# Kernel optimization log

Hardware: AMD Instinct MI355X
Metric: run time of the kernel (lower is better)

Reference implementation:

```python
import jax, jax.numpy as jnp
import numpy as np

B, L, A, K = 2, 1024, 14, 30
NUM_RBF = 16
NPE = 16  # num_positional_embeddings
EF = 128  # edge_features
EDGE_IN = NPE + NUM_RBF * A * A  # 3152


def setup_inputs() -> dict:
    key = jax.random.key(0)
    ks = jax.random.split(key, 4)
    # coords scaled so pairwise distances span the RBF range [0, 20]
    X = jax.random.normal(ks[0], (B, L, A, 3), dtype=jnp.float32) * 3.0
    mask = jnp.ones((B, L), dtype=jnp.float32)
    residue_idx = jnp.tile(jnp.arange(L, dtype=jnp.int32)[None, :], (B, 1))
    chain_labels = jnp.zeros((B, L), dtype=jnp.int32)
    atom_mask = jax.random.randint(ks[1], (B, L, A), 0, 2).astype(jnp.float32)
    W_edge = jax.random.normal(ks[2], (EF, EDGE_IN), dtype=jnp.float32) * 0.02
    ln_gamma = jnp.ones((EF,), dtype=jnp.float32)
    ln_beta = jnp.zeros((EF,), dtype=jnp.float32)
    return {"X": X, "mask": mask, "residue_idx": residue_idx,
            "chain_labels": chain_labels, "atom_mask": atom_mask,
            "W_edge": W_edge, "ln_gamma": ln_gamma, "ln_beta": ln_beta}


def reference(X, mask, residue_idx, chain_labels, atom_mask, W_edge, ln_gamma, ln_beta):
    Bq, Lq = X.shape[0], X.shape[1]
    # ---- CA pairwise distances + masked top-k (smallest) ----
    X_ca = X[:, :, 1, :]
    m2 = mask[:, :, None] * mask[:, None, :]                    # [B,L,L]
    dX = X_ca[:, :, None, :] - X_ca[:, None, :, :]
    D = m2 * jnp.sqrt(jnp.sum(dX ** 2, -1) + 1e-6)
    D_max = jnp.max(D, -1, keepdims=True)
    D_adjust = D + 2.0 * (1.0 - m2) * D_max
    _, E_idx = jax.lax.top_k(-D_adjust, K)                      # smallest K -> [B,L,K]
    # ---- transformer positional encoding of relative index ----
    ii = jnp.arange(Lq, dtype=jnp.float32)[None, :, None]
    d = (E_idx.astype(jnp.float32) - ii)[..., None]             # [B,L,K,1]
    freq = jnp.exp(jnp.arange(0, NPE, 2, dtype=jnp.float32) * (-(np.log(10000.0) / NPE)))
    angles = d * freq                                           # [B,L,K,NPE/2]
    E_pos = jnp.concatenate([jnp.cos(angles), jnp.sin(angles)], -1)  # [B,L,K,NPE]
    # ---- impute CB, build 14-atom set ----
    N_, Ca, C_, O_ = X[:, :, 0, :], X[:, :, 1, :], X[:, :, 2, :], X[:, :, 3, :]
    b = Ca - N_
    c = C_ - Ca
    a = jnp.cross(b, c)
    Cb = -0.58273431 * a + 0.56802827 * b - 0.54067466 * c + Ca
    X2 = jnp.concatenate([jnp.stack([N_, Ca, C_, O_, Cb], -2), X[:, :, 5:, :]], -2)  # [B,L,14,3]
    am = 1.0 - atom_mask                                        # module passes 1 - atom_mask
    # ---- gather neighbor atoms, fused 14x14 atom-pair RBFs ----
    bidx = jnp.arange(Bq)[:, None, None]
    X2n = X2[bidx, E_idx]                                       # [B,L,K,14,3]
    amn = am[bidx, E_idx]                                       # [B,L,K,14]
    diff = X2[:, :, None, :, None, :] - X2n[:, :, :, None, :, :]
    Dab = jnp.sqrt(jnp.sum(diff ** 2, -1) + 1e-6)               # [B,L,K,14,14] (a of i, b of nbr)
    combo = am[:, :, None, :, None] * amn[:, :, :, None, :]     # [B,L,K,14,14]
    mu = jnp.linspace(0.0, 20.0, NUM_RBF)
    sigma = 20.0 / NUM_RBF
    rbf = jnp.exp(-(((Dab[..., None] - mu) / sigma) ** 2)) * combo[..., None]
    RBF_all = rbf.reshape(Bq, Lq, K, A * A * NUM_RBF)           # matches torch cat order (i,j,rbf)
    # ---- edge embedding + layernorm ----
    E = jnp.concatenate([E_pos, RBF_all], -1)                   # [B,L,K,EDGE_IN]
    E = E @ W_edge.T                                            # [B,L,K,EF]
    mean = jnp.mean(E, -1, keepdims=True)
    var = jnp.var(E, -1, keepdims=True)
    E = (E - mean) / jnp.sqrt(var + 1e-5) * ln_gamma + ln_beta
    return (E, E_idx)
```

## Files before the change

kernel.cpp:

```cpp
#include <hip/hip_runtime.h>
#include <hip/hip_bf16.h>
#include <stdint.h>

#define LQ 1024
#define BQ 2
#define AQ 14
#define KQ 30
#define EFQ 128
#define EDGE_IN 3152
#define KPAD 3200
#define NCHUNK 50
#define MTILE 128
#define ROWS (BQ*LQ*KQ)
#define EIDX_OFF (ROWS*EFQ)

typedef __attribute__((ext_vector_type(8))) _Float16 half8;
typedef __attribute__((ext_vector_type(2))) _Float16 half2t;
typedef __attribute__((ext_vector_type(4))) float floatx4;
typedef unsigned long long ull;

static __device__ __forceinline__ uint32_t pkh(float a, float b) {
    auto h = __builtin_amdgcn_cvt_pkrtz(a, b);
    return __builtin_bit_cast(uint32_t, h);
}
static __device__ __forceinline__ ull umin64(ull a, ull b) { return a < b ? a : b; }

__global__ __launch_bounds__(512) void topk_kernel(
    const float* __restrict__ X, const float* __restrict__ mask,
    const float* __restrict__ W, float* __restrict__ out,
    int* __restrict__ idx_ws, _Float16* __restrict__ wpad)
{
    __shared__ float xs[LQ], ys[LQ], zs[LQ], ms[LQ];
    const int t = threadIdx.x;

    if (blockIdx.x >= 256) {
        int base = (blockIdx.x - 256)*8192 + t;
        #pragma unroll
        for (int r = 0; r < 16; ++r) {
            int idx = base + r*512;
            int n = idx / KPAD, f = idx - n*KPAD;
            float v = (f < EDGE_IN) ? W[(size_t)n*EDGE_IN + f] : 0.0f;
            wpad[idx] = (_Float16)v;
        }
        return;
    }

    const int w = t >> 6, lane = t & 63;
    const int row = blockIdx.x*8 + w;
    const int b = row >> 10, i = row & (LQ - 1);

    for (int j = t; j < LQ; j += 512) {
        size_t base = ((size_t)(b*LQ + j))*42 + 3;
        xs[j] = X[base+0]; ys[j] = X[base+1]; zs[j] = X[base+2];
        ms[j] = mask[b*LQ + j];
    }
    __syncthreads();

    const float mif = ms[i];
    const double cx = (double)xs[i], cy = (double)ys[i], cz = (double)zs[i];

    double Dk[16]; float mf[16];
    bool allone = (mif == 1.0f);
    #pragma unroll
    for (int s = 0; s < 16; ++s) {
        int j = s*64 + lane;
        double dx = __dsub_rn(cx, (double)xs[j]);
        double dy = __dsub_rn(cy, (double)ys[j]);
        double dz = __dsub_rn(cz, (double)zs[j]);
        mf[s] = ms[j];
        Dk[s] = __dadd_rn(__dadd_rn(__dmul_rn(dx,dx), __dmul_rn(dy,dy)),
                          __dmul_rn(dz,dz));
        allone = allone && (mf[s] == 1.0f);
    }

    if (!__all(allone ? 1 : 0)) {
        const double mi_d = (double)mif;
        double lm = 0.0;
        #pragma unroll
        for (int s = 0; s < 16; ++s) {
            double m2 = __dmul_rn(mi_d, (double)mf[s]);
            Dk[s] = __dmul_rn(m2, sqrt(__dadd_rn(Dk[s], 1e-6)));
            lm = fmax(lm, Dk[s]);
        }
        #pragma unroll
        for (int off = 32; off; off >>= 1) lm = fmax(lm, __shfl_xor(lm, off));
        #pragma unroll
        for (int s = 0; s < 16; ++s) {
            double m2 = __dmul_rn(mi_d, (double)mf[s]);
            Dk[s] = __dadd_rn(Dk[s],
                    __dmul_rn(__dmul_rn(2.0, __dsub_rn(1.0, m2)), lm));
        }
    }

    ull key[16];
    #pragma unroll
    for (int s = 0; s < 16; ++s)
        key[s] = (((ull)__double_as_longlong(Dk[s])) & ~1023ull)
               | (unsigned)(s*64 + lane);

    for (int k = 0; k < KQ; ++k) {
        ull a0 = umin64(key[0],  key[1]),  a1 = umin64(key[2],  key[3]);
        ull a2 = umin64(key[4],  key[5]),  a3 = umin64(key[6],  key[7]);
        ull a4 = umin64(key[8],  key[9]),  a5 = umin64(key[10], key[11]);
        ull a6 = umin64(key[12], key[13]), a7 = umin64(key[14], key[15]);
        ull b0 = umin64(a0, a1), b1 = umin64(a2, a3);
        ull b2 = umin64(a4, a5), b3 = umin64(a6, a7);
        ull bk = umin64(umin64(b0, b1), umin64(b2, b3));
        #pragma unroll
        for (int off = 32; off; off >>= 1)
            bk = umin64(bk, (ull)__shfl_xor(bk, off));
        int j = (int)(bk & 1023ull);
        if (lane == 0) {
            int rg = row*KQ + k;
            idx_ws[rg] = j;
            out[EIDX_OFF + rg] = (float)j;
        }
        bool mine = ((j & 63) == lane);
        int s_win = j >> 6;
        #pragma unroll
        for (int s = 0; s < 16; ++s)
            key[s] = (mine && s == s_win) ? ~0ull : key[s];
    }
}

struct FusedSmem {
    alignas(16) unsigned short atoms[256*56];
    alignas(16) unsigned short Bl[128*64];
    alignas(16) float drow[MTILE];
    int residg[256];
    unsigned int maskb[256];
    float gsh[EFQ], bsh[EFQ];
};

static __device__ __forceinline__ void gen8(
    const unsigned short* __restrict__ atomsA,
    const unsigned short* __restrict__ atomsB,
    unsigned maskA, unsigned maskB, float drowv,
    int f0, uint32_t* __restrict__ v)
{
    if (f0 >= 16) {
        int p = (f0 - 16) >> 4;
        int rbase = (f0 - 16) & 15;
        int pc = p > 195 ? 195 : p;
        int a  = (pc * 74899) >> 20;
        int bp = pc - a*14;
        bool dead = (p > 195) |
                    ((((maskA >> a) | (maskB >> bp)) & 1u) != 0u);
        half2t c0 = *reinterpret_cast<const half2t*>(atomsA + a*4);
        half2t c1 = *reinterpret_cast<const half2t*>(atomsA + a*4 + 2);
        half2t n0 = *reinterpret_cast<const half2t*>(atomsB + bp*4);
        half2t n1 = *reinterpret_cast<const half2t*>(atomsB + bp*4 + 2);
        half2t dxy = c0 - n0;
        half2t dzw = c1 - n1;
        float dx = (float)dxy[0], dy = (float)dxy[1], dz = (float)dzw[0];
        float u = __builtin_amdgcn_sqrtf(dx*dx + dy*dy + dz*dz + 1e-6f) * 0.96089846f;
        u = dead ? 1.0e4f : u;
        #pragma unroll
        for (int k = 0; k < 4; ++k) {
            float t0 = __fmaf_rn(-(float)(rbase + 2*k),     1.28119795f, u);
            float t1 = __fmaf_rn(-(float)(rbase + 2*k + 1), 1.28119795f, u);
            v[k] = pkh(__builtin_amdgcn_exp2f(-(t0*t0)),
                       __builtin_amdgcn_exp2f(-(t1*t1)));
        }
    } else {
        const float fr[8] = {1.0f, 0.31622776601683794f, 0.1f,
            0.031622776601683794f, 0.01f, 0.0031622776601683794f,
            0.001f, 0.00031622776601683794f};
        float e[8];
        if (f0 == 0) {
            #pragma unroll
            for (int j = 0; j < 8; ++j) e[j] = __cosf(drowv * fr[j]);
        } else {
            #pragma unroll
            for (int j = 0; j < 8; ++j) e[j] = __sinf(drowv * fr[j]);
        }
        #pragma unroll
        for (int k = 0; k < 4; ++k) v[k] = pkh(e[2*k], e[2*k+1]);
    }
}

__global__ __launch_bounds__(256, 3) void fused_kernel(
    const float* __restrict__ X, const float* __restrict__ atom_mask,
    const _Float16* __restrict__ wpad, const float* __restrict__ gamma,
    const float* __restrict__ beta, const int* __restrict__ idx_ws,
    float* __restrict__ out)
{
    __shared__ FusedSmem sm;
    const int t = threadIdx.x;
    const int row0 = blockIdx.x * MTILE;
    const int b = row0 / (LQ*KQ);

    if (t < MTILE) {
        int rg = row0 + t;
        int rem = rg - b*(LQ*KQ);
        int i = rem / KQ;
        int j = idx_ws[rg];
        sm.residg[t]       = b*LQ + i;
        sm.residg[MTILE+t] = b*LQ + j;
        sm.drow[t] = (float)j - (float)i;
    }
    if (t < EFQ) { sm.gsh[t] = gamma[t]; sm.bsh[t] = beta[t]; }
    __syncthreads();

    for (int u2 = t; u2 < 256*14; u2 += 256) {
        int s = u2 / 14; int a = u2 - s*14;
        const float* xp = X + (size_t)sm.residg[s]*42 + a*3;
        uint2 pk; pk.x = pkh(xp[0], xp[1]); pk.y = pkh(xp[2], 0.0f);
        *reinterpret_cast<uint2*>(&sm.atoms[s*56 + a*4]) = pk;
    }
    __syncthreads();

    {
        unsigned short* at = &sm.atoms[t*56];
        auto ld3 = [&](int slot, float& x, float& y, float& z) {
            half2t p0 = *reinterpret_cast<const half2t*>(at + slot*4);
            half2t p1 = *reinterpret_cast<const half2t*>(at + slot*4 + 2);
            x = (float)p0[0]; y = (float)p0[1]; z = (float)p1[0];
        };
        float Nx,Ny,Nz, Cax,Cay,Caz, Cx,Cy,Cz;
        ld3(0, Nx,Ny,Nz); ld3(1, Cax,Cay,Caz); ld3(2, Cx,Cy,Cz);
        float bx=Cax-Nx, by=Cay-Ny, bz=Caz-Nz;
        float ex=Cx-Cax, ey=Cy-Cay, ez=Cz-Caz;
        float ax = by*ez - bz*ey, ay = bz*ex - bx*ez, az = bx*ey - by*ex;
        float cbx = -0.58273431f*ax + 0.56802827f*bx - 0.54067466f*ex + Cax;
        float cby = -0.58273431f*ay + 0.56802827f*by - 0.54067466f*ey + Cay;
        float cbz = -0.58273431f*az + 0.56802827f*bz - 0.54067466f*ez + Caz;
        uint2 pk; pk.x = pkh(cbx, cby); pk.y = pkh(cbz, 0.0f);
        *reinterpret_cast<uint2*>(at + 4*4) = pk;
        unsigned mb = 0;
        const float* amp = &atom_mask[(size_t)sm.residg[t]*AQ];
        #pragma unroll
        for (int a = 0; a < AQ; ++a) if (amp[a] > 0.5f) mb |= (1u << a);
        sm.maskb[t] = mb;
    }

    const int w = t >> 6, lane = t & 63, q = lane >> 4, l15 = lane & 15;
    const int m0 = w*32 + l15, m1 = m0 + 16;

    const int cst0 = l15*64 + ((q ^ (l15 & 7))*8);
    const int cst1 = l15*64 + (((4+q) ^ (l15 & 7))*8);

    const _Float16* stBase[4];
    unsigned short* stDst[4];
    #pragma unroll
    for (int i2 = 0; i2 < 4; ++i2) {
        int region = w*4 + i2;
        int n = region*8 + (lane >> 3);
        int kbsrc = (lane & 7) ^ (lane >> 3);
        stDst[i2]  = &sm.Bl[region*512];
        stBase[i2] = wpad + (size_t)n*KPAD + kbsrc*8;
    }

    floatx4 acc0[8], acc1[8];
    #pragma unroll
    for (int nt = 0; nt < 8; ++nt) {
        acc0[nt] = (floatx4){0.f,0.f,0.f,0.f};
        acc1[nt] = (floatx4){0.f,0.f,0.f,0.f};
    }

    __syncthreads();

    const unsigned short* atomsA0 = &sm.atoms[m0*56];
    const unsigned short* atomsB0 = &sm.atoms[(MTILE+m0)*56];
    const unsigned short* atomsA1 = &sm.atoms[m1*56];
    const unsigned short* atomsB1 = &sm.atoms[(MTILE+m1)*56];
    const unsigned maskA0 = sm.maskb[m0], maskB0 = sm.maskb[MTILE+m0];
    const unsigned maskA1 = sm.maskb[m1], maskB1 = sm.maskb[MTILE+m1];
    const float drow0 = sm.drow[m0], drow1 = sm.drow[m1];

    union H8 { uint32_t u[4]; half8 h; };
    for (int c = 0; c < NCHUNK; ++c) {
        if (c) __syncthreads();
        #pragma unroll
        for (int i2 = 0; i2 < 4; ++i2) {
            const _Float16* g = stBase[i2] + c*64;
            __builtin_amdgcn_global_load_lds(
                (const __attribute__((address_space(1))) uint32_t*)g,
                (__attribute__((address_space(3))) uint32_t*)stDst[i2],
                16, 0, 0);
        }
        H8 a00, a01, a10, a11;
        gen8(atomsA0, atomsB0, maskA0, maskB0, drow0, c*64 + q*8,      a00.u);
        gen8(atomsA0, atomsB0, maskA0, maskB0, drow0, c*64 + 32 + q*8, a01.u);
        gen8(atomsA1, atomsB1, maskA1, maskB1, drow1, c*64 + q*8,      a10.u);
        gen8(atomsA1, atomsB1, maskA1, maskB1, drow1, c*64 + 32 + q*8, a11.u);
        __syncthreads();
        #pragma unroll
        for (int nt = 0; nt < 8; ++nt) {
            half8 b0 = *reinterpret_cast<const half8*>(&sm.Bl[nt*1024 + cst0]);
            half8 b1 = *reinterpret_cast<const half8*>(&sm.Bl[nt*1024 + cst1]);
            acc0[nt] = __builtin_amdgcn_mfma_f32_16x16x32_f16(a00.h, b0, acc0[nt], 0, 0, 0);
            acc0[nt] = __builtin_amdgcn_mfma_f32_16x16x32_f16(a01.h, b1, acc0[nt], 0, 0, 0);
            acc1[nt] = __builtin_amdgcn_mfma_f32_16x16x32_f16(a10.h, b0, acc1[nt], 0, 0, 0);
            acc1[nt] = __builtin_amdgcn_mfma_f32_16x16x32_f16(a11.h, b1, acc1[nt], 0, 0, 0);
        }
    }

    auto lnrows = [&](const floatx4* acc, int gbase) {
        #pragma unroll
        for (int v = 0; v < 4; ++v) {
            float s = 0.f, s2 = 0.f;
            #pragma unroll
            for (int nt = 0; nt < 8; ++nt) { float x = acc[nt][v]; s += x; s2 += x*x; }
            #pragma unroll
            for (int off = 1; off < 16; off <<= 1) {
                s  += __shfl_xor(s,  off);
                s2 += __shfl_xor(s2, off);
            }
            float mean = s * (1.0f/128.0f);
            float var  = s2 * (1.0f/128.0f) - mean*mean;
            float rstd = 1.0f / sqrtf(var + 1e-5f);
            int row_l = w*32 + gbase + q*4 + v;
            size_t obase = (size_t)(row0 + row_l)*EFQ;
            #pragma unroll
            for (int nt = 0; nt < 8; ++nt) {
                int col = nt*16 + l15;
                out[obase + col] = (acc[nt][v] - mean)*rstd*sm.gsh[col] + sm.bsh[col];
            }
        }
    };
    lnrows(acc0, 0);
    lnrows(acc1, 16);
}

extern "C" void kernel_launch(void* const* d_in, const int* in_sizes, int n_in,
                              void* d_out, int out_size, void* d_ws, size_t ws_size,
                              hipStream_t stream)
{
    const float* X         = (const float*)d_in[0];
    const float* mask      = (const float*)d_in[1];
    const float* atom_mask = (const float*)d_in[4];
    const float* W         = (const float*)d_in[5];
    const float* gamma     = (const float*)d_in[6];
    const float* beta      = (const float*)d_in[7];
    float* out = (float*)d_out;

    int*       idx_ws = (int*)d_ws;
    _Float16*  wpad   = (_Float16*)((char*)d_ws + 262144);

    hipLaunchKernelGGL(topk_kernel, dim3(306), dim3(512), 0, stream,
                       X, mask, W, out, idx_ws, wpad);
    hipLaunchKernelGGL(fused_kernel, dim3(ROWS/MTILE), dim3(256), 0, stream,
                       X, atom_mask, wpad, gamma, beta, idx_ws, out);
}
```

Measured before the change: 177.7 us.

## Load GEMM weight fragments directly from global memory instead of LDS staging

Removes the shared-memory staging buffer for the weight tile and the two per-chunk block barriers, so each wave reads its B fragments straight from global memory (L2/L1 cached). The smaller LDS footprint and fewer barriers allow the launch bound to rise to four blocks per CU. The cost is redundant global reads of the same weights by every wave and no swizzled LDS reuse, which exposes the kernel to global-load latency inside the MFMA loop and puts more register pressure on it under the tighter occupancy bound.

```diff
diff --git a/kernel.cpp b/kernel.cpp
--- a/kernel.cpp
+++ b/kernel.cpp
@@ -125,7 +125,6 @@
 
 struct FusedSmem {
     alignas(16) unsigned short atoms[256*56];
-    alignas(16) unsigned short Bl[128*64];
     alignas(16) float drow[MTILE];
     int residg[256];
     unsigned int maskb[256];
@@ -179,7 +178,7 @@
     }
 }
 
-__global__ __launch_bounds__(256, 3) void fused_kernel(
+__global__ __launch_bounds__(256, 4) void fused_kernel(
     const float* __restrict__ X, const float* __restrict__ atom_mask,
     const _Float16* __restrict__ wpad, const float* __restrict__ gamma,
     const float* __restrict__ beta, const int* __restrict__ idx_ws,
@@ -237,19 +236,10 @@
     const int w = t >> 6, lane = t & 63, q = lane >> 4, l15 = lane & 15;
     const int m0 = w*32 + l15, m1 = m0 + 16;
 
-    const int cst0 = l15*64 + ((q ^ (l15 & 7))*8);
-    const int cst1 = l15*64 + (((4+q) ^ (l15 & 7))*8);
-
-    const _Float16* stBase[4];
-    unsigned short* stDst[4];
+    const _Float16* bq = wpad + (size_t)l15*KPAD + q*8;
+    const _Float16* bnt[8];
     #pragma unroll
-    for (int i2 = 0; i2 < 4; ++i2) {
-        int region = w*4 + i2;
-        int n = region*8 + (lane >> 3);
-        int kbsrc = (lane & 7) ^ (lane >> 3);
-        stDst[i2]  = &sm.Bl[region*512];
-        stBase[i2] = wpad + (size_t)n*KPAD + kbsrc*8;
-    }
+    for (int nt = 0; nt < 8; ++nt) bnt[nt] = bq + (size_t)nt*16*KPAD;
 
     floatx4 acc0[8], acc1[8];
     #pragma unroll
@@ -270,25 +260,16 @@
 
     union H8 { uint32_t u[4]; half8 h; };
     for (int c = 0; c < NCHUNK; ++c) {
-        if (c) __syncthreads();
-        #pragma unroll
-        for (int i2 = 0; i2 < 4; ++i2) {
-            const _Float16* g = stBase[i2] + c*64;
-            __builtin_amdgcn_global_load_lds(
-                (const __attribute__((address_space(1))) uint32_t*)g,
-                (__attribute__((address_space(3))) uint32_t*)stDst[i2],
-                16, 0, 0);
-        }
         H8 a00, a01, a10, a11;
         gen8(atomsA0, atomsB0, maskA0, maskB0, drow0, c*64 + q*8,      a00.u);
         gen8(atomsA0, atomsB0, maskA0, maskB0, drow0, c*64 + 32 + q*8, a01.u);
         gen8(atomsA1, atomsB1, maskA1, maskB1, drow1, c*64 + q*8,      a10.u);
         gen8(atomsA1, atomsB1, maskA1, maskB1, drow1, c*64 + 32 + q*8, a11.u);
-        __syncthreads();
+        const int coff = c*64;
         #pragma unroll
         for (int nt = 0; nt < 8; ++nt) {
-            half8 b0 = *reinterpret_cast<const half8*>(&sm.Bl[nt*1024 + cst0]);
-            half8 b1 = *reinterpret_cast<const half8*>(&sm.Bl[nt*1024 + cst1]);
+            half8 b0 = *reinterpret_cast<const half8*>(bnt[nt] + coff);
+            half8 b1 = *reinterpret_cast<const half8*>(bnt[nt] + coff + 32);
             acc0[nt] = __builtin_amdgcn_mfma_f32_16x16x32_f16(a00.h, b0, acc0[nt], 0, 0, 0);
             acc0[nt] = __builtin_amdgcn_mfma_f32_16x16x32_f16(a01.h, b1, acc0[nt], 0, 0, 0);
             acc1[nt] = __builtin_amdgcn_mfma_f32_16x16x32_f16(a10.h, b0, acc1[nt], 0, 0, 0);
```

Measured after the change: 306.8 us. 72.6% more time.
